# Kernel optimization log

Hardware: AMD Instinct MI355X
Metric: run time of the kernel (lower is better)

## Reference

```python
import jax, jax.numpy as jnp
import numpy as np

DIM = 256
N_PATCHES = 2048
N_HEADS = 8
BATCH = 2


def setup_inputs() -> dict:
    key = jax.random.key(0)
    ks = jax.random.split(key, 8)
    d = DIM
    s = d ** -0.5
    return {
        "x": jax.random.normal(ks[0], (BATCH, N_PATCHES, d), dtype=jnp.float32),
        # weights stored (in_features, out_features) so y = x @ W + b
        "W_qk": jax.random.normal(ks[1], (d, 2 * d), dtype=jnp.float32) * s,
        "W_v": jax.random.normal(ks[2], (d, d), dtype=jnp.float32) * s,
        "W_proj": jax.random.normal(ks[3], (d, d), dtype=jnp.float32) * s,
        "b_proj": jnp.zeros((d,), dtype=jnp.float32),
        "W_pos": jax.random.normal(ks[4], (2, N_HEADS), dtype=jnp.float32) * 0.5,
        "b_pos": jnp.zeros((N_HEADS,), dtype=jnp.float32),
        "gating": jnp.ones((N_HEADS,), dtype=jnp.float32),
    }


def reference(x, W_qk, W_v, W_proj, b_proj, W_pos, b_pos, gating):
    B, N, C = x.shape
    H = gating.shape[0]
    Dh = C // H
    scale = Dh ** -0.5

    # content attention: q @ k^T softmax
    qk = (x @ W_qk).reshape(B, N, 2, H, Dh)
    q = jnp.transpose(qk[:, :, 0], (0, 2, 1, 3))  # [B,H,N,Dh]
    k = jnp.transpose(qk[:, :, 1], (0, 2, 1, 3))
    patch_score = jax.nn.softmax(jnp.einsum("bhnd,bhmd->bhnm", q, k) * scale, axis=-1)

    # positional attention from relative indices (d, |d|) -> per-head score
    idx = jnp.arange(N, dtype=jnp.float32)
    rel = idx[:, None] - idx[None, :]                      # [N,N]
    rel_feat = jnp.stack([rel, jnp.abs(rel)], axis=-1)     # [N,N,2]
    pos = rel_feat @ W_pos + b_pos                         # [N,N,H]
    pos_score = jax.nn.softmax(jnp.transpose(pos, (2, 0, 1)), axis=-1)  # [H,N,N]

    g = jax.nn.sigmoid(gating)[None, :, None, None]        # [1,H,1,1]
    attn = (1.0 - g) * patch_score + g * pos_score[None]   # [B,H,N,N]
    attn = attn / jnp.sum(attn, axis=-1, keepdims=True)

    v = jnp.transpose((x @ W_v).reshape(B, N, H, Dh), (0, 2, 1, 3))  # [B,H,N,Dh]
    out = jnp.einsum("bhnm,bhmd->bhnd", attn, v)
    out = jnp.transpose(out, (0, 2, 1, 3)).reshape(B, N, C)
    return out @ W_proj + b_proj
```

## Files before the change

kernel.cpp:

```cpp
#include <hip/hip_runtime.h>
#include <hip/hip_bf16.h>

#define DIM 256
#define NP 2048
#define NH 8
#define BATCH 2
#define DH 32

typedef __attribute__((ext_vector_type(8))) short bshort8;
typedef __attribute__((ext_vector_type(4))) short bshort4;
typedef __attribute__((ext_vector_type(4))) float f32x4;

#define LOG2E 1.44269504f
#define QSCALE (0.17677669529663687f * LOG2E)

union U16B { uint4 u; bshort8 s8; __hip_bfloat16 h[8]; };
union U8B  { uint2 u; bshort4 s4; __hip_bfloat16 h[4]; };

__device__ __forceinline__ float fexp2(float x) { return __builtin_amdgcn_exp2f(x); }
__device__ __forceinline__ unsigned packbf(float hi, float lo) {
    return __builtin_amdgcn_perm(__float_as_uint(hi), __float_as_uint(lo), 0x07060302u);
}

__device__ __forceinline__ int lds_addr(int row, int colg) {
    return row * 256 + (((colg ^ (row & 7)) & 31) << 3);
}

__global__ __launch_bounds__(256) void prep_kernel(
    const float* __restrict__ Wqk,
    const float* __restrict__ Wv,
    const float* __restrict__ Wproj,
    __hip_bfloat16* __restrict__ WT) {
    const int t = threadIdx.x;
    const int blk = blockIdx.x;
    __shared__ float ts[64][65];
    const int ct = blk >> 2, k0 = (blk & 3) * 64;
    const int c0 = ct * 64;
    const float* src; int ldw, cs0; float scl = 1.0f;
    if (ct < 8)       { src = Wqk;   ldw = 512; cs0 = c0;      if (ct < 4) scl = QSCALE; }
    else if (ct < 12) { src = Wv;    ldw = 256; cs0 = c0 - 512; }
    else              { src = Wproj; ldw = 256; cs0 = c0 - 768; }
    const int cc = t & 63, tq = t >> 6;
#pragma unroll
    for (int j = 0; j < 16; j++) {
        int kk = tq * 16 + j;
        ts[kk][cc] = src[(size_t)(k0 + kk) * ldw + cs0 + cc];
    }
    __syncthreads();
    const int kk2 = t & 63;
#pragma unroll
    for (int j = 0; j < 16; j++) {
        int cc2 = tq * 16 + j;
        WT[(size_t)(c0 + cc2) * 256 + k0 + kk2] = __float2bfloat16(ts[kk2][cc2] * scl);
    }
}

__global__ __launch_bounds__(256) void qkv_mfma(
    const float* __restrict__ x,
    const __hip_bfloat16* __restrict__ WT,
    __hip_bfloat16* __restrict__ q,
    __hip_bfloat16* __restrict__ k,
    __hip_bfloat16* __restrict__ vT) {
    __shared__ __align__(16) __hip_bfloat16 As[64 * 256];
    __shared__ __align__(16) __hip_bfloat16 Bs[64 * 256];
    const int t = threadIdx.x, lane = t & 63, wvid = t >> 6;
    const int l15 = lane & 15, l4 = lane >> 4;
    const int m0 = blockIdx.x * 64;
    const int nb0 = blockIdx.y * 64;
    const int nc = nb0 + wvid * 16 + l15;

#pragma unroll
    for (int j = 0; j < 8; j++) {
        const int flat = j * 2048 + t * 8;
        const int row = flat >> 8, colg = (flat >> 3) & 31;
        float4 f0 = *(const float4*)(x + (size_t)m0 * 256 + flat);
        float4 f1 = *(const float4*)(x + (size_t)m0 * 256 + flat + 4);
        U16B a;
        a.h[0] = __float2bfloat16(f0.x); a.h[1] = __float2bfloat16(f0.y);
        a.h[2] = __float2bfloat16(f0.z); a.h[3] = __float2bfloat16(f0.w);
        a.h[4] = __float2bfloat16(f1.x); a.h[5] = __float2bfloat16(f1.y);
        a.h[6] = __float2bfloat16(f1.z); a.h[7] = __float2bfloat16(f1.w);
        *(uint4*)&As[lds_addr(row, colg)] = a.u;
        *(uint4*)&Bs[lds_addr(row, colg)] = *(const uint4*)(WT + (size_t)nb0 * 256 + flat);
    }
    __syncthreads();

    f32x4 acc[4] = {{0.f,0.f,0.f,0.f},{0.f,0.f,0.f,0.f},{0.f,0.f,0.f,0.f},{0.f,0.f,0.f,0.f}};
#pragma unroll
    for (int kk = 0; kk < 8; kk++) {
        const int colg = kk * 4 + l4;
        U16B bw; bw.u = *(const uint4*)&Bs[lds_addr(wvid * 16 + l15, colg)];
#pragma unroll
        for (int mt = 0; mt < 4; mt++) {
            U16B ax; ax.u = *(const uint4*)&As[lds_addr(mt * 16 + l15, colg)];
            acc[mt] = __builtin_amdgcn_mfma_f32_16x16x32_bf16(ax.s8, bw.s8, acc[mt], 0, 0, 0);
        }
    }

    if (nb0 < 256) {
        const int h = nc >> 5, d = nc & 31;
#pragma unroll
        for (int mt = 0; mt < 4; mt++)
#pragma unroll
            for (int r = 0; r < 4; r++) {
                int tok = m0 + mt * 16 + l4 * 4 + r;
                int b = tok >> 11, n = tok & (NP - 1);
                q[((size_t)(b * NH + h) * NP + n) * DH + d] = __float2bfloat16(acc[mt][r]);
            }
    } else if (nb0 < 512) {
        const int c = nc - 256, h = c >> 5, d = c & 31;
#pragma unroll
        for (int mt = 0; mt < 4; mt++)
#pragma unroll
            for (int r = 0; r < 4; r++) {
                int tok = m0 + mt * 16 + l4 * 4 + r;
                int b = tok >> 11, n = tok & (NP - 1);
                k[((size_t)(b * NH + h) * NP + n) * DH + d] = __float2bfloat16(acc[mt][r]);
            }
    } else {
        const int c = nc - 512;
        const int b = m0 >> 11;
#pragma unroll
        for (int mt = 0; mt < 4; mt++) {
            int tokn = (m0 & (NP - 1)) + mt * 16 + l4 * 4;
            U8B vv;
#pragma unroll
            for (int r = 0; r < 4; r++) vv.h[r] = __float2bfloat16(acc[mt][r]);
            *(uint2*)(vT + (size_t)(b * 256 + c) * NP + tokn) = vv.u;
        }
    }
}

__global__ __launch_bounds__(512, 4) void attn_kernel(
    const __hip_bfloat16* __restrict__ qg,
    const __hip_bfloat16* __restrict__ kg,
    const __hip_bfloat16* __restrict__ vTg,
    const float* __restrict__ Wpos,
    const float* __restrict__ bpos,
    const float* __restrict__ gating,
    __hip_bfloat16* __restrict__ ao) {
    __shared__ __align__(16) __hip_bfloat16 Kt[2][2][64][40];
    __shared__ __align__(16) __hip_bfloat16 Vt[2][2][32][68];
    __shared__ float cmb[4][2][32][16];
    __shared__ float cls[4][2][16];

    const int t = threadIdx.x;
    const int lane = t & 63, wvid = t >> 6;
    const int l15 = lane & 15, l4 = lane >> 4;
    const int qt = wvid & 3, kh = wvid >> 2;
    const int bh = blockIdx.x >> 5, qb = blockIdx.x & 31;
    const int h = bh & (NH - 1), b = bh >> 3;
    const int q0 = qb * 64 + qt * 16;
    const int myq = q0 + l15;

    const int st_ = t & 255;
    const int kstart = kh * 1024;
    const __hip_bfloat16* kptr = kg + (size_t)bh * NP * DH + (size_t)(kstart + (st_ >> 2)) * DH + (st_ & 3) * 8;
    const __hip_bfloat16* vptr = vTg + ((size_t)bh * DH + (st_ >> 3)) * NP + kstart + (st_ & 7) * 8;

    uint4 kreg = *(const uint4*)kptr;
    uint4 vreg = *(const uint4*)vptr;
    *(uint4*)&Kt[kh][0][st_ >> 2][(st_ & 3) * 8] = kreg;
    *(uint2*)&Vt[kh][0][st_ >> 3][(st_ & 7) * 8]     = make_uint2(vreg.x, vreg.y);
    *(uint2*)&Vt[kh][0][st_ >> 3][(st_ & 7) * 8 + 4] = make_uint2(vreg.z, vreg.w);

    const float w0 = Wpos[h] * LOG2E;
    const float w1 = Wpos[NH + h] * LOG2E;
    const float g = 1.0f / (1.0f + __expf(-gating[h]));
    const float nf = (float)myq;
    const float pmax = fmaxf(0.f, fmaxf((w0 + w1) * nf, (w1 - w0) * (2047.0f - nf)));
    const float npmax = -pmax;
    const float rA = fexp2(-(w0 + w1));
    const float rB = fexp2(w1 - w0);

    U16B qv;
    qv.u = *(const uint4*)(qg + ((size_t)bh * NP + myq) * DH + l4 * 8);

    __syncthreads();

    f32x4 os0 = {0.f,0.f,0.f,0.f}, os1 = {0.f,0.f,0.f,0.f};
    f32x4 op0 = {0.f,0.f,0.f,0.f}, op1 = {0.f,0.f,0.f,0.f};
    float ls = 0.f, lp = 0.f;

    for (int it = 0; it < 16; ++it) {
        const int cur = it & 1, nxt = cur ^ 1;

        if (it < 15) {
            kreg = *(const uint4*)(kptr + (size_t)(it + 1) * 64 * DH);
            vreg = *(const uint4*)(vptr + (it + 1) * 64);
        }

        f32x4 st4[4];
#pragma unroll
        for (int kt = 0; kt < 4; kt++) {
            U16B kf; kf.u = *(const uint4*)&Kt[kh][cur][kt * 16 + l15][l4 * 8];
            st4[kt] = __builtin_amdgcn_mfma_f32_16x16x32_bf16(
                kf.s8, qv.s8, (f32x4){0.f,0.f,0.f,0.f}, 0, 0, 0);
        }

        U8B vfr[8];
#pragma unroll
        for (int vh = 0; vh < 2; vh++)
#pragma unroll
            for (int kt = 0; kt < 4; kt++)
                vfr[vh * 4 + kt].u = *(const uint2*)&Vt[kh][cur][vh * 16 + l15][kt * 16 + l4 * 4];

        const int kb0 = kstart + it * 64;
#pragma unroll
        for (int kt = 0; kt < 4; kt++) {
            float es0 = fexp2(st4[kt][0]), es1 = fexp2(st4[kt][1]);
            float es2 = fexp2(st4[kt][2]), es3 = fexp2(st4[kt][3]);
            ls += (es0 + es1) + (es2 + es3);
            const float d0 = nf - (float)(kb0 + kt * 16 + l4 * 4);
            float ep0 = fexp2(fmaf(w1, fabsf(d0), fmaf(w0, d0, npmax)));
            float ep1 = ep0 * ((d0 >= 1.f) ? rA : rB);
            float ep2 = ep1 * ((d0 >= 2.f) ? rA : rB);
            float ep3 = ep2 * ((d0 >= 3.f) ? rA : rB);
            lp += (ep0 + ep1) + (ep2 + ep3);
            U8B pc, pp;
            pc.u.x = packbf(es1, es0); pc.u.y = packbf(es3, es2);
            pp.u.x = packbf(ep1, ep0); pp.u.y = packbf(ep3, ep2);
            os0 = __builtin_amdgcn_mfma_f32_16x16x16bf16_1k(vfr[kt].s4,     pc.s4, os0, 0, 0, 0);
            os1 = __builtin_amdgcn_mfma_f32_16x16x16bf16_1k(vfr[4 + kt].s4, pc.s4, os1, 0, 0, 0);
            op0 = __builtin_amdgcn_mfma_f32_16x16x16bf16_1k(vfr[kt].s4,     pp.s4, op0, 0, 0, 0);
            op1 = __builtin_amdgcn_mfma_f32_16x16x16bf16_1k(vfr[4 + kt].s4, pp.s4, op1, 0, 0, 0);
        }

        if (it < 15) {
            *(uint4*)&Kt[kh][nxt][st_ >> 2][(st_ & 3) * 8] = kreg;
            *(uint2*)&Vt[kh][nxt][st_ >> 3][(st_ & 7) * 8]     = make_uint2(vreg.x, vreg.y);
            *(uint2*)&Vt[kh][nxt][st_ >> 3][(st_ & 7) * 8 + 4] = make_uint2(vreg.z, vreg.w);
        }
        __syncthreads();
    }

    ls += __shfl_xor(ls, 16, 64); ls += __shfl_xor(ls, 32, 64);
    lp += __shfl_xor(lp, 16, 64); lp += __shfl_xor(lp, 32, 64);

    if (kh == 1) {
#pragma unroll
        for (int r = 0; r < 4; r++) {
            cmb[qt][0][l4 * 4 + r][l15]      = os0[r];
            cmb[qt][0][16 + l4 * 4 + r][l15] = os1[r];
            cmb[qt][1][l4 * 4 + r][l15]      = op0[r];
            cmb[qt][1][16 + l4 * 4 + r][l15] = op1[r];
        }
        if (l4 == 0) { cls[qt][0][l15] = ls; cls[qt][1][l15] = lp; }
    }
    __syncthreads();
    if (kh == 0) {
        ls += cls[qt][0][l15]; lp += cls[qt][1][l15];
        const float cs = (1.0f - g) / ls;
        const float cp = g / lp;
        const size_t orow = ((size_t)b * NP + myq) * DIM + h * DH;
        U8B o0, o1;
#pragma unroll
        for (int r = 0; r < 4; r++) {
            o0.h[r] = __float2bfloat16(cs * (os0[r] + cmb[qt][0][l4 * 4 + r][l15]) +
                                       cp * (op0[r] + cmb[qt][1][l4 * 4 + r][l15]));
            o1.h[r] = __float2bfloat16(cs * (os1[r] + cmb[qt][0][16 + l4 * 4 + r][l15]) +
                                       cp * (op1[r] + cmb[qt][1][16 + l4 * 4 + r][l15]));
        }
        *(uint2*)(ao + orow + l4 * 4)      = o0.u;
        *(uint2*)(ao + orow + 16 + l4 * 4) = o1.u;
    }
}

__global__ __launch_bounds__(256) void proj_mfma(
    const __hip_bfloat16* __restrict__ ao,
    const __hip_bfloat16* __restrict__ WT,
    const float* __restrict__ bias,
    float* __restrict__ out) {
    __shared__ __align__(16) __hip_bfloat16 As[64 * 256];
    __shared__ __align__(16) __hip_bfloat16 Bs[64 * 256];
    const int t = threadIdx.x, lane = t & 63, wvid = t >> 6;
    const int l15 = lane & 15, l4 = lane >> 4;
    const int m0 = blockIdx.x * 64;
    const int nb0 = blockIdx.y * 64;
    const int nc = nb0 + wvid * 16 + l15;

#pragma unroll
    for (int j = 0; j < 8; j++) {
        const int flat = j * 2048 + t * 8;
        const int row = flat >> 8, colg = (flat >> 3) & 31;
        *(uint4*)&As[lds_addr(row, colg)] = *(const uint4*)(ao + (size_t)m0 * 256 + flat);
        *(uint4*)&Bs[lds_addr(row, colg)] = *(const uint4*)(WT + (size_t)(768 + nb0) * 256 + flat);
    }
    __syncthreads();

    f32x4 acc[4] = {{0.f,0.f,0.f,0.f},{0.f,0.f,0.f,0.f},{0.f,0.f,0.f,0.f},{0.f,0.f,0.f,0.f}};
#pragma unroll
    for (int kk = 0; kk < 8; kk++) {
        const int colg = kk * 4 + l4;
        U16B bw; bw.u = *(const uint4*)&Bs[lds_addr(wvid * 16 + l15, colg)];
#pragma unroll
        for (int mt = 0; mt < 4; mt++) {
            U16B ax; ax.u = *(const uint4*)&As[lds_addr(mt * 16 + l15, colg)];
            acc[mt] = __builtin_amdgcn_mfma_f32_16x16x32_bf16(ax.s8, bw.s8, acc[mt], 0, 0, 0);
        }
    }

    const float bb = bias[nc];
#pragma unroll
    for (int mt = 0; mt < 4; mt++)
#pragma unroll
        for (int r = 0; r < 4; r++) {
            int tok = m0 + mt * 16 + l4 * 4 + r;
            out[(size_t)tok * 256 + nc] = acc[mt][r] + bb;
        }
}

extern "C" void kernel_launch(void* const* d_in, const int* in_sizes, int n_in,
                              void* d_out, int out_size, void* d_ws, size_t ws_size,
                              hipStream_t stream) {
    const float* x      = (const float*)d_in[0];
    const float* Wqk    = (const float*)d_in[1];
    const float* Wv     = (const float*)d_in[2];
    const float* Wproj  = (const float*)d_in[3];
    const float* bproj  = (const float*)d_in[4];
    const float* Wpos   = (const float*)d_in[5];
    const float* bpos   = (const float*)d_in[6];
    const float* gating = (const float*)d_in[7];
    float* out = (float*)d_out;

    const size_t nElem = (size_t)BATCH * NP * DIM;
    char* w = (char*)d_ws;
    __hip_bfloat16* WT = (__hip_bfloat16*)w;
    __hip_bfloat16* q  = WT + 262144;
    __hip_bfloat16* k  = q + nElem;
    __hip_bfloat16* vT = k + nElem;
    __hip_bfloat16* ao = vT + nElem;

    prep_kernel<<<64, 256, 0, stream>>>(Wqk, Wv, Wproj, WT);
    qkv_mfma<<<dim3(64, 12), 256, 0, stream>>>(x, WT, q, k, vT);
    attn_kernel<<<BATCH * NH * (NP / 64), 512, 0, stream>>>(q, k, vT, Wpos, bpos, gating, ao);
    proj_mfma<<<dim3(64, 4), 256, 0, stream>>>(ao, WT, bproj, out);
}
```

Measured before the change: 107.4 us.

## Store V in MFMA fragment layout and read K/V directly from global

The QKV kernel now writes V pre-arranged in the per-lane MFMA fragment order, and stages Q/K through LDS so it can write them with coalesced 16-byte stores. The attention kernel drops its LDS double-buffering of K and V along with the per-iteration __syncthreads, and instead loads fragments straight from global memory (through L2/cache), unrolling the loop by two. This removes LDS traffic and barriers, but makes every wave issue its own global loads, so redundant reads across the four query-tile waves now depend on cache hits and latency hiding.

```diff
diff --git a/kernel.cpp b/kernel.cpp
--- a/kernel.cpp
+++ b/kernel.cpp
@@ -60,14 +60,13 @@
     const __hip_bfloat16* __restrict__ WT,
     __hip_bfloat16* __restrict__ q,
     __hip_bfloat16* __restrict__ k,
-    __hip_bfloat16* __restrict__ vT) {
+    __hip_bfloat16* __restrict__ vF) {
     __shared__ __align__(16) __hip_bfloat16 As[64 * 256];
     __shared__ __align__(16) __hip_bfloat16 Bs[64 * 256];
     const int t = threadIdx.x, lane = t & 63, wvid = t >> 6;
     const int l15 = lane & 15, l4 = lane >> 4;
     const int m0 = blockIdx.x * 64;
     const int nb0 = blockIdx.y * 64;
-    const int nc = nb0 + wvid * 16 + l15;
 
 #pragma unroll
     for (int j = 0; j < 8; j++) {
@@ -97,36 +96,38 @@
         }
     }
 
-    if (nb0 < 256) {
-        const int h = nc >> 5, d = nc & 31;
+    if (nb0 < 512) {
+        __syncthreads();
+        __hip_bfloat16* Tr = As;
 #pragma unroll
         for (int mt = 0; mt < 4; mt++)
 #pragma unroll
-            for (int r = 0; r < 4; r++) {
-                int tok = m0 + mt * 16 + l4 * 4 + r;
-                int b = tok >> 11, n = tok & (NP - 1);
-                q[((size_t)(b * NH + h) * NP + n) * DH + d] = __float2bfloat16(acc[mt][r]);
-            }
-    } else if (nb0 < 512) {
-        const int c = nc - 256, h = c >> 5, d = c & 31;
-#pragma unroll
-        for (int mt = 0; mt < 4; mt++)
-#pragma unroll
-            for (int r = 0; r < 4; r++) {
-                int tok = m0 + mt * 16 + l4 * 4 + r;
-                int b = tok >> 11, n = tok & (NP - 1);
-                k[((size_t)(b * NH + h) * NP + n) * DH + d] = __float2bfloat16(acc[mt][r]);
-            }
+            for (int r = 0; r < 4; r++)
+                Tr[(mt * 16 + l4 * 4 + r) * 72 + wvid * 16 + l15] = __float2bfloat16(acc[mt][r]);
+        __syncthreads();
+        const int hh = t >> 7, row = (t >> 1) & 63, part = t & 1;
+        const bool isq = (nb0 < 256);
+        const int cc = (isq ? nb0 : nb0 - 256) + hh * 32;
+        const int hOut = cc >> 5;
+        const int tok = m0 + row;
+        const int b = tok >> 11, n = tok & (NP - 1);
+        __hip_bfloat16* dst = (isq ? q : k) + ((size_t)(b * NH + hOut) * NP + n) * DH + part * 16;
+        uint4 w0 = *(const uint4*)&Tr[row * 72 + hh * 32 + part * 16];
+        uint4 w1 = *(const uint4*)&Tr[row * 72 + hh * 32 + part * 16 + 8];
+        *(uint4*)dst = w0;
+        *(uint4*)(dst + 8) = w1;
     } else {
-        const int c = nc - 512;
+        const int cbase = (nb0 - 512) + wvid * 16;
+        const int h = cbase >> 5;
+        const int vh = (cbase >> 4) & 1;
         const int b = m0 >> 11;
 #pragma unroll
         for (int mt = 0; mt < 4; mt++) {
-            int tokn = (m0 & (NP - 1)) + mt * 16 + l4 * 4;
+            const int kt = ((m0 & (NP - 1)) >> 4) + mt;
             U8B vv;
 #pragma unroll
             for (int r = 0; r < 4; r++) vv.h[r] = __float2bfloat16(acc[mt][r]);
-            *(uint2*)(vT + (size_t)(b * 256 + c) * NP + tokn) = vv.u;
+            *(uint2*)(vF + ((((size_t)((b * NH + h) * 128 + kt)) * 2 + vh) * 64 + lane) * 4) = vv.u;
         }
     }
 }
@@ -134,13 +135,11 @@
 __global__ __launch_bounds__(512, 4) void attn_kernel(
     const __hip_bfloat16* __restrict__ qg,
     const __hip_bfloat16* __restrict__ kg,
-    const __hip_bfloat16* __restrict__ vTg,
+    const __hip_bfloat16* __restrict__ vF,
     const float* __restrict__ Wpos,
     const float* __restrict__ bpos,
     const float* __restrict__ gating,
     __hip_bfloat16* __restrict__ ao) {
-    __shared__ __align__(16) __hip_bfloat16 Kt[2][2][64][40];
-    __shared__ __align__(16) __hip_bfloat16 Vt[2][2][32][68];
     __shared__ float cmb[4][2][32][16];
     __shared__ float cls[4][2][16];
 
@@ -153,17 +152,6 @@
     const int q0 = qb * 64 + qt * 16;
     const int myq = q0 + l15;
 
-    const int st_ = t & 255;
-    const int kstart = kh * 1024;
-    const __hip_bfloat16* kptr = kg + (size_t)bh * NP * DH + (size_t)(kstart + (st_ >> 2)) * DH + (st_ & 3) * 8;
-    const __hip_bfloat16* vptr = vTg + ((size_t)bh * DH + (st_ >> 3)) * NP + kstart + (st_ & 7) * 8;
-
-    uint4 kreg = *(const uint4*)kptr;
-    uint4 vreg = *(const uint4*)vptr;
-    *(uint4*)&Kt[kh][0][st_ >> 2][(st_ & 3) * 8] = kreg;
-    *(uint2*)&Vt[kh][0][st_ >> 3][(st_ & 7) * 8]     = make_uint2(vreg.x, vreg.y);
-    *(uint2*)&Vt[kh][0][st_ >> 3][(st_ & 7) * 8 + 4] = make_uint2(vreg.z, vreg.w);
-
     const float w0 = Wpos[h] * LOG2E;
     const float w1 = Wpos[NH + h] * LOG2E;
     const float g = 1.0f / (1.0f + __expf(-gating[h]));
@@ -176,36 +164,37 @@
     U16B qv;
     qv.u = *(const uint4*)(qg + ((size_t)bh * NP + myq) * DH + l4 * 8);
 
-    __syncthreads();
+    const __hip_bfloat16* kbase = kg + (size_t)bh * NP * DH;
+    const __hip_bfloat16* vbase = vF + (size_t)bh * 128 * 2 * 256;
+    const int kstart = kh * 1024;
 
     f32x4 os0 = {0.f,0.f,0.f,0.f}, os1 = {0.f,0.f,0.f,0.f};
     f32x4 op0 = {0.f,0.f,0.f,0.f}, op1 = {0.f,0.f,0.f,0.f};
     float ls = 0.f, lp = 0.f;
 
+#pragma unroll 2
     for (int it = 0; it < 16; ++it) {
-        const int cur = it & 1, nxt = cur ^ 1;
-
-        if (it < 15) {
-            kreg = *(const uint4*)(kptr + (size_t)(it + 1) * 64 * DH);
-            vreg = *(const uint4*)(vptr + (it + 1) * 64);
-        }
+        const int kb0 = kstart + it * 64;
+        const int kt0 = kb0 >> 4;
+
+        U8B vfr[8];
+#pragma unroll
+        for (int ktl = 0; ktl < 4; ktl++)
+#pragma unroll
+            for (int vh = 0; vh < 2; vh++)
+                vfr[vh * 4 + ktl].u = *(const uint2*)(vbase +
+                    (((size_t)(kt0 + ktl) * 2 + vh) * 64 + lane) * 4);
+        U16B kf[4];
+#pragma unroll
+        for (int kt = 0; kt < 4; kt++)
+            kf[kt].u = *(const uint4*)(kbase + (size_t)(kb0 + kt * 16 + l15) * DH + l4 * 8);
 
         f32x4 st4[4];
 #pragma unroll
-        for (int kt = 0; kt < 4; kt++) {
-            U16B kf; kf.u = *(const uint4*)&Kt[kh][cur][kt * 16 + l15][l4 * 8];
+        for (int kt = 0; kt < 4; kt++)
             st4[kt] = __builtin_amdgcn_mfma_f32_16x16x32_bf16(
-                kf.s8, qv.s8, (f32x4){0.f,0.f,0.f,0.f}, 0, 0, 0);
-        }
-
-        U8B vfr[8];
-#pragma unroll
-        for (int vh = 0; vh < 2; vh++)
-#pragma unroll
-            for (int kt = 0; kt < 4; kt++)
-                vfr[vh * 4 + kt].u = *(const uint2*)&Vt[kh][cur][vh * 16 + l15][kt * 16 + l4 * 4];
-
-        const int kb0 = kstart + it * 64;
+                kf[kt].s8, qv.s8, (f32x4){0.f,0.f,0.f,0.f}, 0, 0, 0);
+
 #pragma unroll
         for (int kt = 0; kt < 4; kt++) {
             float es0 = fexp2(st4[kt][0]), es1 = fexp2(st4[kt][1]);
@@ -225,13 +214,6 @@
             op0 = __builtin_amdgcn_mfma_f32_16x16x16bf16_1k(vfr[kt].s4,     pp.s4, op0, 0, 0, 0);
             op1 = __builtin_amdgcn_mfma_f32_16x16x16bf16_1k(vfr[4 + kt].s4, pp.s4, op1, 0, 0, 0);
         }
-
-        if (it < 15) {
-            *(uint4*)&Kt[kh][nxt][st_ >> 2][(st_ & 3) * 8] = kreg;
-            *(uint2*)&Vt[kh][nxt][st_ >> 3][(st_ & 7) * 8]     = make_uint2(vreg.x, vreg.y);
-            *(uint2*)&Vt[kh][nxt][st_ >> 3][(st_ & 7) * 8 + 4] = make_uint2(vreg.z, vreg.w);
-        }
-        __syncthreads();
     }
 
     ls += __shfl_xor(ls, 16, 64); ls += __shfl_xor(ls, 32, 64);
@@ -328,11 +310,11 @@
     __hip_bfloat16* WT = (__hip_bfloat16*)w;
     __hip_bfloat16* q  = WT + 262144;
     __hip_bfloat16* k  = q + nElem;
-    __hip_bfloat16* vT = k + nElem;
-    __hip_bfloat16* ao = vT + nElem;
+    __hip_bfloat16* vF = k + nElem;
+    __hip_bfloat16* ao = vF + nElem;
 
     prep_kernel<<<64, 256, 0, stream>>>(Wqk, Wv, Wproj, WT);
-    qkv_mfma<<<dim3(64, 12), 256, 0, stream>>>(x, WT, q, k, vT);
-    attn_kernel<<<BATCH * NH * (NP / 64), 512, 0, stream>>>(q, k, vT, Wpos, bpos, gating, ao);
+    qkv_mfma<<<dim3(64, 12), 256, 0, stream>>>(x, WT, q, k, vF);
+    attn_kernel<<<BATCH * NH * (NP / 64), 512, 0, stream>>>(q, k, vF, Wpos, bpos, gating, ao);
     proj_mfma<<<dim3(64, 4), 256, 0, stream>>>(ao, WT, bproj, out);
 }
```

Measured after the change: 115.9 us. 7.9% more time.
